# Kernel tuning notes

Measured on AMD Instinct MI355X. Metric: run time of the kernel, lower is better.

## Reference

```python
import jax, jax.numpy as jnp
import numpy as np

D_MODEL = 512
D_INNER = 1024   # expand * d_model
D_STATE = 16
D_CONV = 4
DT_RANK = 32     # ceil(d_model / 16)
BATCH = 8
SEQ = 1024


def _mamba(x, in_w, conv_w, conv_b, xp_w, dt_w, dt_b, A_log, Dp, out_w):
    # x: [B, L, d_model]
    Bb, Ls, _ = x.shape
    u, z = jnp.split(x @ in_w.T, 2, axis=-1)          # each [B, L, d_inner]
    # causal depthwise conv1d, kernel D_CONV, left-padded then truncated to L
    up = jnp.pad(u, ((0, 0), (D_CONV - 1, 0), (0, 0)))
    uc = conv_b + sum(up[:, k:k + Ls, :] * conv_w[:, k] for k in range(D_CONV))
    u = jax.nn.silu(uc)
    dbl = u @ xp_w.T                                   # [B, L, dt_rank+2*d_state]
    dt, Bm, Cm = jnp.split(dbl, [DT_RANK, DT_RANK + D_STATE], axis=-1)
    delta = jax.nn.softplus(dt @ dt_w.T + dt_b)        # [B, L, d_inner]
    A = -jnp.exp(A_log)                                # [d_inner, d_state]

    def step(h, inp):
        d_t, B_t, C_t, u_t = inp                       # [B,di],[B,ds],[B,ds],[B,di]
        h = h * jnp.exp(d_t[..., None] * A) + (d_t * u_t)[..., None] * B_t[:, None, :]
        return h, jnp.einsum('bds,bs->bd', h, C_t)

    h0 = jnp.zeros((Bb, D_INNER, D_STATE), x.dtype)
    xs = tuple(jnp.swapaxes(a, 0, 1) for a in (delta, Bm, Cm, u))
    _, ys = jax.lax.scan(step, h0, xs)                 # ys: [L, B, d_inner]
    y = jnp.swapaxes(ys, 0, 1) + u * Dp
    return (y * jax.nn.silu(z)) @ out_w.T              # [B, L, d_model]


def _params(key):
    ks = jax.random.split(key, 5)
    s = 0.02
    return {
        'in_w': jax.random.normal(ks[0], (2 * D_INNER, D_MODEL)) * s,
        'conv_w': jax.random.normal(ks[1], (D_INNER, D_CONV)) * 0.3,
        'conv_b': jnp.zeros((D_INNER,)),
        'xp_w': jax.random.normal(ks[2], (DT_RANK + 2 * D_STATE, D_INNER)) * s,
        'dt_w': jax.random.normal(ks[3], (D_INNER, DT_RANK)) * (DT_RANK ** -0.5),
        'dt_b': jnp.full((D_INNER,), -4.0),
        'A_log': jnp.log(jnp.tile(jnp.arange(1, D_STATE + 1, dtype=jnp.float32), (D_INNER, 1))),
        'D': jnp.ones((D_INNER,)),
        'out_w': jax.random.normal(ks[4], (D_MODEL, D_INNER)) * s,
    }


def setup_inputs():
    key = jax.random.key(0)
    kx, kf, kb = jax.random.split(key, 3)
    inp = {'x': jax.random.normal(kx, (BATCH, SEQ, D_MODEL), dtype=jnp.float32)}
    for n, v in _params(kf).items():
        inp[n + '_f'] = v
    for n, v in _params(kb).items():
        inp[n + '_b'] = v
    return inp


def reference(x, in_w_f, conv_w_f, conv_b_f, xp_w_f, dt_w_f, dt_b_f, A_log_f, D_f, out_w_f,
              in_w_b, conv_w_b, conv_b_b, xp_w_b, dt_w_b, dt_b_b, A_log_b, D_b, out_w_b):
    fwd = _mamba(x, in_w_f, conv_w_f, conv_b_f, xp_w_f, dt_w_f, dt_b_f, A_log_f, D_f, out_w_f)
    bwd = _mamba(x[:, ::-1, :], in_w_b, conv_w_b, conv_b_b, xp_w_b, dt_w_b, dt_b_b,
                 A_log_b, D_b, out_w_b)[:, ::-1, :]
    return fwd + bwd
```

## Files before the change

kernel.cpp:

```cpp
#include <hip/hip_runtime.h>
#include <math.h>

#define BATCH 8
#define SEQ 1024
#define D_MODEL 512
#define D_INNER 1024
#define D_STATE 16
#define DT_RANK 32
#define NROWS (BATCH * SEQ)
#define CH 64
#define CL 16
#define USLAB 8388608l

typedef short short8 __attribute__((ext_vector_type(8)));
typedef float f32x4 __attribute__((ext_vector_type(4)));

__device__ __forceinline__ float sigmoidf_(float x) { return 1.f / (1.f + __expf(-x)); }

__device__ __forceinline__ float softplus_(float v) {
  return (v > 20.f) ? v : __logf(1.f + __expf(v));
}

__device__ __forceinline__ ushort f2b(float f) {
  uint u = __float_as_uint(f);
  return (ushort)((u + 0x7FFFu + ((u >> 16) & 1u)) >> 16);
}
__device__ __forceinline__ float b2f(ushort u) {
  return __uint_as_float(((uint)u) << 16);
}

__device__ __forceinline__ void gload16(const ushort* g, const ushort* l) {
  __builtin_amdgcn_global_load_lds(
      (const __attribute__((address_space(1))) void*)g,
      (__attribute__((address_space(3))) void*)l, 16, 0, 0);
}

__device__ __forceinline__ int revrow(int m) {
  return (m & ~1023) | (1023 - (m & 1023));
}

__global__ __launch_bounds__(512, 2) void inproj256(
    const ushort* __restrict__ A, int lda,
    const ushort* __restrict__ B, int ldb,
    ushort* __restrict__ Cu, ushort* __restrict__ Cz,
    int K)
{
  __shared__ ushort As[3][256 * 32];
  __shared__ ushort Bs[3][256 * 32];
  const int tid = threadIdx.x;
  const int w = tid >> 6, lane = tid & 63;

  const int nwg = gridDim.x * gridDim.y;
  int bid = blockIdx.y * gridDim.x + blockIdx.x;
  int wgid = (bid & 7) * (nwg >> 3) + (bid >> 3);
  const int bm = (wgid / gridDim.x) * 256;
  const int bn = (wgid % gridDim.x) * 256;

  const int wr = w >> 2, wc = w & 3;
  const int rw0 = wr * 128, cw0 = wc * 64;
  const int srow = w * 16 + (lane >> 2);
  const int scol = (((lane & 3) ^ ((lane >> 3) & 3)) << 3);
  const int rchunk = (((lane >> 4) ^ (((lane & 15) >> 1) & 3)) << 3);

  f32x4 acc[8][4] = {};

  auto stageA = [&](int buf, int k0, int half) {
    int gm = bm + half * 128 + srow;
    gload16(A + (long)gm * lda + k0 + scol, &As[buf][(half * 128 + w * 16) * 32]);
  };
  auto stageB = [&](int buf, int k0, int half) {
    int gn = bn + half * 128 + srow;
    gload16(B + (long)gn * ldb + k0 + scol, &Bs[buf][(half * 128 + w * 16) * 32]);
  };

  const int NT = K >> 5;
  stageA(0, 0, 0); stageA(0, 0, 1); stageB(0, 0, 0); stageB(0, 0, 1);
  stageA(1, 32, 0); stageA(1, 32, 1); stageB(1, 32, 0); stageB(1, 32, 1);
  asm volatile("s_waitcnt vmcnt(4)" ::: "memory");
  __builtin_amdgcn_s_barrier();

  int buf = 0;
  for (int t = 0; t < NT; ++t) {
    const int kf = (t + 2) << 5;
    const int sbuf = (buf >= 1) ? buf - 1 : buf + 2;
    short8 a0[4], b0[4];
#pragma unroll
    for (int i = 0; i < 4; ++i)
      a0[i] = *(const short8*)&As[buf][(rw0 + i * 16 + (lane & 15)) * 32 + rchunk];
#pragma unroll
    for (int j = 0; j < 4; ++j)
      b0[j] = *(const short8*)&Bs[buf][(cw0 + j * 16 + (lane & 15)) * 32 + rchunk];
    if (t + 2 < NT) { stageA(sbuf, kf, 0); stageA(sbuf, kf, 1); }
    __builtin_amdgcn_s_barrier();
    __builtin_amdgcn_s_setprio(1);
#pragma unroll
    for (int i = 0; i < 4; ++i)
#pragma unroll
      for (int j = 0; j < 4; ++j)
        acc[i][j] = __builtin_amdgcn_mfma_f32_16x16x32_bf16(a0[i], b0[j], acc[i][j], 0, 0, 0);
    __builtin_amdgcn_s_setprio(0);
    __builtin_amdgcn_s_barrier();
    short8 a1[4];
#pragma unroll
    for (int i = 0; i < 4; ++i)
      a1[i] = *(const short8*)&As[buf][(rw0 + 64 + i * 16 + (lane & 15)) * 32 + rchunk];
    if (t + 2 < NT) {
      stageB(sbuf, kf, 0); stageB(sbuf, kf, 1);
      asm volatile("s_waitcnt vmcnt(4)" ::: "memory");
    } else if (t + 1 < NT) {
      asm volatile("s_waitcnt vmcnt(0)" ::: "memory");
    }
    __builtin_amdgcn_s_barrier();
    __builtin_amdgcn_s_setprio(1);
#pragma unroll
    for (int i = 0; i < 4; ++i)
#pragma unroll
      for (int j = 0; j < 4; ++j)
        acc[4 + i][j] = __builtin_amdgcn_mfma_f32_16x16x32_bf16(a1[i], b0[j], acc[4 + i][j], 0, 0, 0);
    __builtin_amdgcn_s_setprio(0);
    __builtin_amdgcn_s_barrier();
    buf = (buf == 2) ? 0 : buf + 1;
  }

  const int bdir = bn >> 11;
  const int bz = ((bn & 2047) >= 1024);
  const int bncol = bn & 1023;
  ushort* Cp = (bz ? Cz : Cu) + (long)bdir * USLAB;
  ushort* scr = &As[0][0] + w * 1024;

#pragma unroll
  for (int i = 0; i < 8; ++i) {
#pragma unroll
    for (int r = 0; r < 4; ++r)
#pragma unroll
      for (int j = 0; j < 4; ++j) {
        float v = acc[i][j][r];
        if (bz) v = v * sigmoidf_(v);
        scr[((lane >> 4) * 4 + r) * 64 + j * 16 + (lane & 15)] = f2b(v);
      }
#pragma unroll
    for (int q = 0; q < 2; ++q) {
      int r16 = (lane >> 3) + q * 8;
      short8 pk = *(const short8*)&scr[r16 * 64 + (lane & 7) * 8];
      int m = bm + rw0 + i * 16 + r16;
      int row = bdir ? revrow(m) : m;
      *(short8*)&Cp[(long)row * 1024 + bncol + cw0 + (lane & 7) * 8] = pk;
    }
  }
}

template<int BM, int BN, int RW, int CW, int EPI, int DUALK, int MDIAG>
__global__ __launch_bounds__(256) void gemm_bf16(
    const ushort* __restrict__ A, int lda, const ushort* __restrict__ A2,
    const ushort* __restrict__ B, int ldb, const ushort* __restrict__ B2,
    float* __restrict__ Cf, ushort* __restrict__ Cb, ushort* __restrict__ Cb2,
    int ldc, int K, const float* __restrict__ bias, const float* __restrict__ bias2,
    int b_stride, int revC, int accumC)
{
  constexpr int MI = BM / RW / 16;
  constexpr int NJ = BN / CW / 16;
  __shared__ ushort As[2][BM * 32];
  __shared__ ushort Bs[2][BN * 32];
  const int tid = threadIdx.x;
  const int w = tid >> 6, lane = tid & 63;

  const int nwg = gridDim.x * gridDim.y;
  int bid = blockIdx.y * gridDim.x + blockIdx.x;
  int wgid = (bid & 7) * (nwg >> 3) + (bid >> 3);
  const int bm = (wgid / gridDim.x) * BM;
  const int bn = (wgid % gridDim.x) * BN;

  if (MDIAG) {
    int mdir = (bm >= NROWS) ? 1 : 0;
    B += mdir * b_stride;
    if (mdir) bias = bias2;
  }

  const int rw0 = (w / CW) * (MI * 16);
  const int cw0 = (w % CW) * (NJ * 16);
  const int srow = w * 16 + (lane >> 2);
  const int scol = (((lane & 3) ^ ((lane >> 3) & 3)) << 3);
  const int rchunk = (((lane >> 4) ^ (((lane & 15) >> 1) & 3)) << 3);

  f32x4 acc[MI][NJ] = {};

  auto stage = [&](int buf, int k0) {
    const ushort* Ap = A;
    const ushort* Bp = B;
    int kc = k0;
    bool hi = false;
    if (DUALK && k0 >= (K >> 1)) { Ap = A2; Bp = B2; kc = k0 - (K >> 1); hi = true; }
#pragma unroll
    for (int it = 0; it < BM / 64; ++it) {
      int gm = bm + it * 64 + srow;
      int arow = (DUALK && hi) ? revrow(gm) : gm;
      gload16(Ap + (long)arow * lda + kc + scol, &As[buf][(it * 64 + w * 16) * 32]);
    }
#pragma unroll
    for (int it = 0; it < BN / 64; ++it) {
      int gn = bn + it * 64 + srow;
      gload16(Bp + (long)gn * ldb + kc + scol, &Bs[buf][(it * 64 + w * 16) * 32]);
    }
  };

  stage(0, 0);
  __syncthreads();

  for (int k0 = 0; k0 < K; k0 += 32) {
    int cur = (k0 >> 5) & 1;
    if (k0 + 32 < K) stage(cur ^ 1, k0 + 32);
    short8 a[MI], b[NJ];
#pragma unroll
    for (int i = 0; i < MI; ++i)
      a[i] = *(const short8*)&As[cur][(rw0 + i * 16 + (lane & 15)) * 32 + rchunk];
#pragma unroll
    for (int j = 0; j < NJ; ++j)
      b[j] = *(const short8*)&Bs[cur][(cw0 + j * 16 + (lane & 15)) * 32 + rchunk];
#pragma unroll
    for (int i = 0; i < MI; ++i)
#pragma unroll
      for (int j = 0; j < NJ; ++j)
        acc[i][j] = __builtin_amdgcn_mfma_f32_16x16x32_bf16(a[i], b[j], acc[i][j], 0, 0, 0);
    __syncthreads();
  }

  if (EPI == 1) {
    ushort* scr = &As[0][0] + w * 1024;
#pragma unroll
    for (int i = 0; i < MI; ++i) {
#pragma unroll
      for (int r = 0; r < 4; ++r)
#pragma unroll
        for (int j = 0; j < NJ; ++j) {
          int n = bn + cw0 + j * 16 + (lane & 15);
          float v = softplus_(acc[i][j][r] + bias[n]);
          scr[((lane >> 4) * 4 + r) * 64 + j * 16 + (lane & 15)] = f2b(v);
        }
#pragma unroll
      for (int q = 0; q < 2; ++q) {
        int r16 = (lane >> 3) + q * 8;
        short8 pk = *(const short8*)&scr[r16 * 64 + (lane & 7) * 8];
        int m = bm + rw0 + i * 16 + r16;
        *(short8*)&Cb[(long)m * ldc + bn + cw0 + (lane & 7) * 8] = pk;
      }
    }
  } else {
#pragma unroll
    for (int i = 0; i < MI; ++i)
#pragma unroll
      for (int r = 0; r < 4; ++r) {
        int m = bm + rw0 + i * 16 + (lane >> 4) * 4 + r;
        int crow = revC ? revrow(m) : m;
#pragma unroll
        for (int j = 0; j < NJ; ++j) {
          int n = bn + cw0 + j * 16 + (lane & 15);
          float v = acc[i][j][r];
          if (EPI == 0) {
            float* p = Cf + (long)crow * ldc + n;
            if (accumC) *p += v; else *p = v;
          } else {
            Cb[(long)crow * ldc + n] = f2b(v);
          }
        }
      }
  }
}

struct Seg { const float4* s; ushort4* d; int n4; int bstart; };
struct ConvArgs { Seg seg[9]; };

__global__ __launch_bounds__(256) void convert_all(ConvArgs a)
{
  int blk = blockIdx.x;
  int i = 0;
#pragma unroll
  for (int k = 1; k < 9; ++k) if (blk >= a.seg[k].bstart) i = k;
  int idx = (blk - a.seg[i].bstart) * 256 + threadIdx.x;
  if (idx >= a.seg[i].n4) return;
  float4 v = a.seg[i].s[idx];
  ushort4 o;
  o.x = f2b(v.x); o.y = f2b(v.y); o.z = f2b(v.z); o.w = f2b(v.w);
  a.seg[i].d[idx] = o;
}

__global__ __launch_bounds__(256) void conv_silu(
    const ushort* __restrict__ u_bf,
    const float* __restrict__ cw_f, const float* __restrict__ cw_b,
    const float* __restrict__ cb_f, const float* __restrict__ cb_b,
    ushort* __restrict__ uc_bf)
{
  long i = (long)blockIdx.x * 256 + threadIdx.x;
  int dir = (int)(i >> 21);
  int r = (int)(i >> 8) & 8191;
  int d0 = ((int)i & 255) << 2;
  int t = r & (SEQ - 1);
  const float* cw = dir ? cw_b : cw_f;
  const float* cb = dir ? cb_b : cb_f;
  const ushort* p = u_bf + dir * USLAB + (long)r * D_INNER + d0;
  ushort4 u0 = *(const ushort4*)p;
  ushort4 u1 = (t >= 1) ? *(const ushort4*)(p - 1024) : ushort4{0, 0, 0, 0};
  ushort4 u2 = (t >= 2) ? *(const ushort4*)(p - 2048) : ushort4{0, 0, 0, 0};
  ushort4 u3 = (t >= 3) ? *(const ushort4*)(p - 3072) : ushort4{0, 0, 0, 0};
  float4 bb = *(const float4*)(cb + d0);
  float ub0[4] = {b2f(u0.x), b2f(u0.y), b2f(u0.z), b2f(u0.w)};
  float ub1[4] = {b2f(u1.x), b2f(u1.y), b2f(u1.z), b2f(u1.w)};
  float ub2[4] = {b2f(u2.x), b2f(u2.y), b2f(u2.z), b2f(u2.w)};
  float ub3[4] = {b2f(u3.x), b2f(u3.y), b2f(u3.z), b2f(u3.w)};
  float bbv[4] = {bb.x, bb.y, bb.z, bb.w};
  ushort ov[4];
#pragma unroll
  for (int j = 0; j < 4; ++j) {
    float4 wj = *(const float4*)(cw + (d0 + j) * 4);
    float acc = bbv[j];
    acc = fmaf(wj.w, ub0[j], acc);
    acc = fmaf(wj.z, ub1[j], acc);
    acc = fmaf(wj.y, ub2[j], acc);
    acc = fmaf(wj.x, ub3[j], acc);
    ov[j] = f2b(acc * sigmoidf_(acc));
  }
  ushort4 o;
  o.x = ov[0]; o.y = ov[1]; o.z = ov[2]; o.w = ov[3];
  *(ushort4*)(uc_bf + dir * USLAB + (long)r * D_INNER + d0) = o;
}

#define EP_FAST(dt, Ep)                                        \
  {                                                            \
    float E1 = __expf(-(dt));                                  \
    float E2 = E1 * E1, E4 = E2 * E2, E8 = E4 * E4;            \
    Ep[0] = E1;  Ep[1] = E2;      Ep[2] = E2 * E1;             \
    Ep[3] = E4;  Ep[4] = E4 * E1; Ep[5] = E4 * E2;             \
    Ep[6] = E4 * Ep[2]; Ep[7] = E8;  Ep[8] = E8 * E1;          \
    Ep[9] = E8 * E2; Ep[10] = E8 * Ep[2]; Ep[11] = E8 * E4;    \
    Ep[12] = E8 * Ep[4]; Ep[13] = E8 * Ep[5];                  \
    Ep[14] = E8 * Ep[6]; Ep[15] = E8 * E8;                     \
  }

__device__ __forceinline__ bool a_is_arange(const float* Ar) {
  bool ok = true;
#pragma unroll
  for (int s = 0; s < D_STATE; ++s)
    ok = ok && (fabsf(Ar[s] + (float)(s + 1)) <= 1e-3f * (float)(s + 1));
  return ok;
}

__global__ __launch_bounds__(256) void scan_partA(
    const ushort* __restrict__ delta_bf,
    const ushort* __restrict__ ucv_bf,
    const ushort* __restrict__ dblb,
    const float* __restrict__ A_log_f, const float* __restrict__ A_log_b,
    ushort* __restrict__ hend,
    float* __restrict__ dtsum_buf)
{
  __shared__ float bc[CL][16];
  long idx = (long)blockIdx.x * 256 + threadIdx.x;
  int d = (int)idx & 1023;
  int c = ((int)idx >> 10) & (CH - 1);
  int b = ((int)idx >> 16) & 7;
  int dir = (int)(idx >> 19);
  const long r0 = (long)b * SEQ + c * CL;
  const ushort* dblp = dblb + (long)dir * NROWS * 64;
  {
    int tt = threadIdx.x >> 4, ss = threadIdx.x & 15;
    bc[tt][ss] = b2f(dblp[(r0 + tt) * 64 + 32 + ss]);
  }
  const float* Alog = dir ? A_log_b : A_log_f;
  const ushort* dp = delta_bf + dir * USLAB;
  const ushort* up = ucv_bf + dir * USLAB;
  float Ar[D_STATE];
#pragma unroll
  for (int s = 0; s < D_STATE; ++s) Ar[s] = -__expf(Alog[d * D_STATE + s]);
  const bool fast = a_is_arange(Ar);
  float h[D_STATE] = {0.f};
  float dtsum = 0.f;
  __syncthreads();

  if (fast) {
    for (int t = 0; t < CL; ++t) {
      long r = r0 + t;
      float dt = b2f(dp[r * 1024 + d]);
      float u  = b2f(up[r * 1024 + d]);
      float du = dt * u;
      dtsum += dt;
      float Ep[16];
      EP_FAST(dt, Ep);
#pragma unroll
      for (int s = 0; s < D_STATE; ++s)
        h[s] = fmaf(h[s], Ep[s], du * bc[t][s]);
    }
  } else {
    for (int t = 0; t < CL; ++t) {
      long r = r0 + t;
      float dt = b2f(dp[r * 1024 + d]);
      float u  = b2f(up[r * 1024 + d]);
      float du = dt * u;
      dtsum += dt;
#pragma unroll
      for (int s = 0; s < D_STATE; ++s)
        h[s] = fmaf(h[s], __expf(dt * Ar[s]), du * bc[t][s]);
    }
  }
  long base = ((long)((dir * 8 + b) * CH + c) * D_STATE) * 1024 + d;
#pragma unroll
  for (int s = 0; s < D_STATE; ++s) hend[base + s * 1024] = f2b(h[s]);
  dtsum_buf[(long)((dir * 8 + b) * CH + c) * 1024 + d] = dtsum;
}

__global__ __launch_bounds__(256) void scan_partB(
    ushort* __restrict__ hend,
    const float* __restrict__ dtsum_buf,
    const float* __restrict__ A_log_f, const float* __restrict__ A_log_b)
{
  long idx = (long)blockIdx.x * 256 + threadIdx.x;
  int d = (int)idx & 1023;
  int s = ((int)idx >> 10) & 15;
  int b = ((int)idx >> 14) & 7;
  int dir = (int)(idx >> 17);
  const float* Alog = dir ? A_log_b : A_log_f;
  float Ars = -__expf(Alog[d * D_STATE + s]);
  float H = 0.f;
  for (int c = 0; c < CH; ++c) {
    long off = ((long)((dir * 8 + b) * CH + c) * D_STATE + s) * 1024 + d;
    float he = b2f(hend[off]);
    float P = __expf(Ars * dtsum_buf[(long)((dir * 8 + b) * CH + c) * 1024 + d]);
    hend[off] = f2b(H);
    H = fmaf(P, H, he);
  }
}

__global__ __launch_bounds__(256) void scan_partC(
    const ushort* __restrict__ delta_bf,
    const ushort* __restrict__ ucv_bf,
    const ushort* __restrict__ dblb,
    const float* __restrict__ A_log_f, const float* __restrict__ A_log_b,
    const float* __restrict__ Dp_f, const float* __restrict__ Dp_b,
    const ushort* __restrict__ zsilu_bf,
    const ushort* __restrict__ hinit,
    ushort* __restrict__ ydz_bf)
{
  __shared__ float bc[CL][32];
  long idx = (long)blockIdx.x * 256 + threadIdx.x;
  int d = (int)idx & 1023;
  int c = ((int)idx >> 10) & (CH - 1);
  int b = ((int)idx >> 16) & 7;
  int dir = (int)(idx >> 19);
  const long r0 = (long)b * SEQ + c * CL;
  const ushort* dblp = dblb + (long)dir * NROWS * 64;
  {
    int tt = threadIdx.x >> 4, cc = (threadIdx.x & 15) * 2;
    ushort2 v = *(const ushort2*)&dblp[(r0 + tt) * 64 + 32 + cc];
    bc[tt][cc] = b2f(v.x); bc[tt][cc + 1] = b2f(v.y);
  }
  const float* Alog = dir ? A_log_b : A_log_f;
  const ushort* dp = delta_bf + dir * USLAB;
  const ushort* up = ucv_bf + dir * USLAB;
  const ushort* zp = zsilu_bf + dir * USLAB;
  ushort* yp = ydz_bf + dir * USLAB;
  float Ar[D_STATE];
#pragma unroll
  for (int s = 0; s < D_STATE; ++s) Ar[s] = -__expf(Alog[d * D_STATE + s]);
  const bool fast = a_is_arange(Ar);
  float h[D_STATE];
  long base = ((long)((dir * 8 + b) * CH + c) * D_STATE) * 1024 + d;
#pragma unroll
  for (int s = 0; s < D_STATE; ++s) h[s] = b2f(hinit[base + s * 1024]);
  float Dd = (dir ? Dp_b : Dp_f)[d];
  __syncthreads();

  if (fast) {
    for (int t = 0; t < CL; ++t) {
      long r = r0 + t;
      float dt = b2f(dp[r * 1024 + d]);
      float u  = b2f(up[r * 1024 + d]);
      float du = dt * u;
      float Ep[16];
      EP_FAST(dt, Ep);
      float y = 0.f;
#pragma unroll
      for (int s = 0; s < D_STATE; ++s) {
        h[s] = fmaf(h[s], Ep[s], du * bc[t][s]);
        y = fmaf(h[s], bc[t][16 + s], y);
      }
      float zs = b2f(zp[r * 1024 + d]);
      float yv = fmaf(u, Dd, y);
      yp[r * 1024 + d] = f2b(yv * zs);
    }
  } else {
    for (int t = 0; t < CL; ++t) {
      long r = r0 + t;
      float dt = b2f(dp[r * 1024 + d]);
      float u  = b2f(up[r * 1024 + d]);
      float du = dt * u;
      float y = 0.f;
#pragma unroll
      for (int s = 0; s < D_STATE; ++s) {
        h[s] = fmaf(h[s], __expf(dt * Ar[s]), du * bc[t][s]);
        y = fmaf(h[s], bc[t][16 + s], y);
      }
      float zs = b2f(zp[r * 1024 + d]);
      float yv = fmaf(u, Dd, y);
      yp[r * 1024 + d] = f2b(yv * zs);
    }
  }
}

extern "C" void kernel_launch(void* const* d_in, const int* in_sizes, int n_in,
                              void* d_out, int out_size, void* d_ws, size_t ws_size,
                              hipStream_t stream)
{
  const float* x = (const float*)d_in[0];
  float* out = (float*)d_out;
  char* ws = (char*)d_ws;
  ushort* zsilu  = (ushort*)(ws);
  ushort* ucv    = (ushort*)(ws + (32ul << 20));
  ushort* u_bf   = (ushort*)(ws + (64ul << 20));
  ushort* hend   = (ushort*)(ws + (96ul << 20));
  float*  dtsum  = (float*)(ws + (128ul << 20));
  ushort* dblb   = (ushort*)(ws + (132ul << 20));
  ushort* out_wb = (ushort*)(ws + (134ul << 20));
  ushort* xbf    = hend;
  ushort* in_wb  = hend + (8ul << 19);
  ushort* xp_wb  = hend + (12ul << 19);
  ushort* dt_wb  = xp_wb + 131072;
  ushort* delta  = u_bf;
  ushort* ydz    = ucv;

  ConvArgs ca;
  int bcur = 0, si = 0;
  auto addseg = [&](const float* s, ushort* d, int nelem) {
    ca.seg[si].s = (const float4*)s; ca.seg[si].d = (ushort4*)d;
    ca.seg[si].n4 = nelem / 4; ca.seg[si].bstart = bcur;
    bcur += (nelem / 4 + 255) / 256; ++si;
  };
  addseg(x, xbf, NROWS * D_MODEL);
  addseg((const float*)d_in[1], in_wb, 2048 * 512);
  addseg((const float*)d_in[10], in_wb + 2048 * 512, 2048 * 512);
  addseg((const float*)d_in[9], out_wb, 512 * 1024);
  addseg((const float*)d_in[18], out_wb + 512 * 1024, 512 * 1024);
  addseg((const float*)d_in[4], xp_wb, 64 * 1024);
  addseg((const float*)d_in[13], xp_wb + 65536, 64 * 1024);
  addseg((const float*)d_in[5], dt_wb, 1024 * 32);
  addseg((const float*)d_in[14], dt_wb + 32768, 1024 * 32);

  dim3 blk(256);
  convert_all<<<dim3(bcur), blk, 0, stream>>>(ca);

  inproj256<<<dim3(4096 / 256, NROWS / 256), dim3(512), 0, stream>>>(
      xbf, D_MODEL, in_wb, D_MODEL, u_bf, zsilu, D_MODEL);
  conv_silu<<<dim3(2 * NROWS), blk, 0, stream>>>(
      u_bf, (const float*)d_in[2], (const float*)d_in[11],
      (const float*)d_in[3], (const float*)d_in[12], ucv);
  gemm_bf16<64, 64, 2, 2, 4, 0, 1><<<dim3(1, 256), blk, 0, stream>>>(
      ucv, D_INNER, nullptr, xp_wb, D_INNER, nullptr,
      nullptr, dblb, nullptr, 64, D_INNER, nullptr, nullptr, 65536, 0, 0);
  gemm_bf16<128, 128, 2, 2, 1, 0, 1><<<dim3(8, 128), blk, 0, stream>>>(
      dblb, 64, nullptr, dt_wb, DT_RANK, nullptr,
      nullptr, delta, nullptr, D_INNER, DT_RANK,
      (const float*)d_in[6], (const float*)d_in[15], 32768, 0, 0);
  const float* Alf = (const float*)d_in[7];
  const float* Alb = (const float*)d_in[16];
  scan_partA<<<dim3(2 * BATCH * CH * 1024 / 256), blk, 0, stream>>>(
      delta, ucv, dblb, Alf, Alb, hend, dtsum);
  scan_partB<<<dim3(2 * BATCH * 16 * 1024 / 256), blk, 0, stream>>>(
      hend, dtsum, Alf, Alb);
  scan_partC<<<dim3(2 * BATCH * CH * 1024 / 256), blk, 0, stream>>>(
      delta, ucv, dblb, Alf, Alb,
      (const float*)d_in[8], (const float*)d_in[17], zsilu, hend, ydz);
  gemm_bf16<128, 128, 2, 2, 0, 1, 0><<<dim3(4, 64), blk, 0, stream>>>(
      ydz, D_INNER, ydz + USLAB, out_wb, D_INNER, out_wb + 512 * 1024,
      out, nullptr, nullptr, D_MODEL, 2 * D_INNER, nullptr, nullptr, 0, 0, 0);
}
```

Before: 254.7 us.

## Fuse x_proj and dt_proj GEMMs into one kernel; widen conv_silu vectors

Adds xdt_kernel, which computes the x_proj GEMM for a 64-row tile, keeps the resulting dt/B/C tile in shared memory, and applies the dt projection with the softplus-plus-bias epilogue in the same kernel. Only B/C columns go to dblb; the dt columns are no longer written to and re-read from global memory, and one launch is saved. conv_silu now handles 8 channels per thread with short8 loads and stores instead of 4. The trade-off is that the fused kernel runs only 256 workgroups, each doing the whole dt projection serially across its 4 waves, which may reduce parallelism compared with the separate 1024-block delta GEMM.

```diff
diff --git a/kernel.cpp b/kernel.cpp
--- a/kernel.cpp
+++ b/kernel.cpp
@@ -149,6 +149,114 @@
   }
 }
 
+__global__ __launch_bounds__(256) void xdt_kernel(
+    const ushort* __restrict__ A,
+    const ushort* __restrict__ xp_w,
+    const ushort* __restrict__ dt_w,
+    const float* __restrict__ dt_b_f, const float* __restrict__ dt_b_b,
+    ushort* __restrict__ dblb,
+    ushort* __restrict__ delta)
+{
+  __shared__ ushort As[2][64 * 32];
+  __shared__ ushort Bs[2][64 * 32];
+  __shared__ ushort dblS[64][72];
+  __shared__ ushort scr[4][1024];
+  const int tid = threadIdx.x;
+  const int w = tid >> 6, lane = tid & 63;
+
+  const int nwg = gridDim.x;
+  int wgid = (blockIdx.x & 7) * (nwg >> 3) + (blockIdx.x >> 3);
+  const int bm = wgid * 64;
+  const int mdir = (bm >= NROWS) ? 1 : 0;
+  const ushort* B = xp_w + mdir * 65536;
+  const ushort* dtw = dt_w + mdir * 32768;
+  const float* dbias = mdir ? dt_b_b : dt_b_f;
+
+  const int rw0 = (w >> 1) * 32;
+  const int cw0 = (w & 1) * 32;
+  const int srow = w * 16 + (lane >> 2);
+  const int scol = (((lane & 3) ^ ((lane >> 3) & 3)) << 3);
+  const int rchunk = (((lane >> 4) ^ (((lane & 15) >> 1) & 3)) << 3);
+
+  f32x4 acc[2][2] = {};
+  auto stage = [&](int buf, int k0) {
+    gload16(A + (long)(bm + srow) * 1024 + k0 + scol, &As[buf][(w * 16) * 32]);
+    gload16(B + (long)srow * 1024 + k0 + scol, &Bs[buf][(w * 16) * 32]);
+  };
+  stage(0, 0);
+  __syncthreads();
+  for (int k0 = 0; k0 < 1024; k0 += 32) {
+    int cur = (k0 >> 5) & 1;
+    if (k0 + 32 < 1024) stage(cur ^ 1, k0 + 32);
+    short8 a[2], b[2];
+#pragma unroll
+    for (int i = 0; i < 2; ++i)
+      a[i] = *(const short8*)&As[cur][(rw0 + i * 16 + (lane & 15)) * 32 + rchunk];
+#pragma unroll
+    for (int j = 0; j < 2; ++j)
+      b[j] = *(const short8*)&Bs[cur][(cw0 + j * 16 + (lane & 15)) * 32 + rchunk];
+#pragma unroll
+    for (int i = 0; i < 2; ++i)
+#pragma unroll
+      for (int j = 0; j < 2; ++j)
+        acc[i][j] = __builtin_amdgcn_mfma_f32_16x16x32_bf16(a[i], b[j], acc[i][j], 0, 0, 0);
+    __syncthreads();
+  }
+
+#pragma unroll
+  for (int i = 0; i < 2; ++i)
+#pragma unroll
+    for (int r = 0; r < 4; ++r)
+#pragma unroll
+      for (int j = 0; j < 2; ++j)
+        dblS[rw0 + i * 16 + (lane >> 4) * 4 + r][cw0 + j * 16 + (lane & 15)] =
+            f2b(acc[i][j][r]);
+  __syncthreads();
+
+  {
+    int row = tid >> 2, cg = tid & 3;
+    short8 pk = *(const short8*)&dblS[row][32 + cg * 8];
+    *(short8*)&dblb[(long)(bm + row) * 64 + 32 + cg * 8] = pk;
+  }
+
+  for (int g = 0; g < 4; ++g) {
+    int n0 = w * 256 + g * 64;
+    short8 a2[4], b2[4];
+#pragma unroll
+    for (int m = 0; m < 4; ++m)
+      a2[m] = *(const short8*)&dblS[m * 16 + (lane & 15)][(lane >> 4) * 8];
+#pragma unroll
+    for (int j = 0; j < 4; ++j)
+      b2[j] = *(const short8*)&dtw[(long)(n0 + j * 16 + (lane & 15)) * 32 + (lane >> 4) * 8];
+    f32x4 acc2[4][4] = {};
+#pragma unroll
+    for (int m = 0; m < 4; ++m)
+#pragma unroll
+      for (int j = 0; j < 4; ++j)
+        acc2[m][j] = __builtin_amdgcn_mfma_f32_16x16x32_bf16(a2[m], b2[j], acc2[m][j], 0, 0, 0);
+    float bv[4];
+#pragma unroll
+    for (int j = 0; j < 4; ++j) bv[j] = dbias[n0 + j * 16 + (lane & 15)];
+#pragma unroll
+    for (int m = 0; m < 4; ++m) {
+#pragma unroll
+      for (int r = 0; r < 4; ++r)
+#pragma unroll
+        for (int j = 0; j < 4; ++j) {
+          float v = softplus_(acc2[m][j][r] + bv[j]);
+          scr[w][((lane >> 4) * 4 + r) * 64 + j * 16 + (lane & 15)] = f2b(v);
+        }
+#pragma unroll
+      for (int q = 0; q < 2; ++q) {
+        int r16 = (lane >> 3) + q * 8;
+        short8 pk = *(const short8*)&scr[w][r16 * 64 + (lane & 7) * 8];
+        int grow = bm + m * 16 + r16;
+        *(short8*)&delta[(long)grow * 1024 + n0 + (lane & 7) * 8] = pk;
+      }
+    }
+  }
+}
+
 template<int BM, int BN, int RW, int CW, int EPI, int DUALK, int MDIAG>
 __global__ __launch_bounds__(256) void gemm_bf16(
     const ushort* __restrict__ A, int lda, const ushort* __restrict__ A2,
@@ -224,46 +332,24 @@
     __syncthreads();
   }
 
-  if (EPI == 1) {
-    ushort* scr = &As[0][0] + w * 1024;
-#pragma unroll
-    for (int i = 0; i < MI; ++i) {
-#pragma unroll
-      for (int r = 0; r < 4; ++r)
-#pragma unroll
-        for (int j = 0; j < NJ; ++j) {
-          int n = bn + cw0 + j * 16 + (lane & 15);
-          float v = softplus_(acc[i][j][r] + bias[n]);
-          scr[((lane >> 4) * 4 + r) * 64 + j * 16 + (lane & 15)] = f2b(v);
-        }
-#pragma unroll
-      for (int q = 0; q < 2; ++q) {
-        int r16 = (lane >> 3) + q * 8;
-        short8 pk = *(const short8*)&scr[r16 * 64 + (lane & 7) * 8];
-        int m = bm + rw0 + i * 16 + r16;
-        *(short8*)&Cb[(long)m * ldc + bn + cw0 + (lane & 7) * 8] = pk;
-      }
-    }
-  } else {
-#pragma unroll
-    for (int i = 0; i < MI; ++i)
-#pragma unroll
-      for (int r = 0; r < 4; ++r) {
-        int m = bm + rw0 + i * 16 + (lane >> 4) * 4 + r;
-        int crow = revC ? revrow(m) : m;
-#pragma unroll
-        for (int j = 0; j < NJ; ++j) {
-          int n = bn + cw0 + j * 16 + (lane & 15);
-          float v = acc[i][j][r];
-          if (EPI == 0) {
-            float* p = Cf + (long)crow * ldc + n;
-            if (accumC) *p += v; else *p = v;
-          } else {
-            Cb[(long)crow * ldc + n] = f2b(v);
-          }
+#pragma unroll
+  for (int i = 0; i < MI; ++i)
+#pragma unroll
+    for (int r = 0; r < 4; ++r) {
+      int m = bm + rw0 + i * 16 + (lane >> 4) * 4 + r;
+      int crow = revC ? revrow(m) : m;
+#pragma unroll
+      for (int j = 0; j < NJ; ++j) {
+        int n = bn + cw0 + j * 16 + (lane & 15);
+        float v = acc[i][j][r];
+        if (EPI == 0) {
+          float* p = Cf + (long)crow * ldc + n;
+          if (accumC) *p += v; else *p = v;
+        } else {
+          Cb[(long)crow * ldc + n] = f2b(v);
         }
       }
-  }
+    }
 }
 
 struct Seg { const float4* s; ushort4* d; int n4; int bstart; };
@@ -290,37 +376,33 @@
     ushort* __restrict__ uc_bf)
 {
   long i = (long)blockIdx.x * 256 + threadIdx.x;
-  int dir = (int)(i >> 21);
-  int r = (int)(i >> 8) & 8191;
-  int d0 = ((int)i & 255) << 2;
+  int dir = (int)(i >> 20);
+  int r = (int)(i >> 7) & 8191;
+  int d0 = ((int)i & 127) << 3;
   int t = r & (SEQ - 1);
   const float* cw = dir ? cw_b : cw_f;
   const float* cb = dir ? cb_b : cb_f;
   const ushort* p = u_bf + dir * USLAB + (long)r * D_INNER + d0;
-  ushort4 u0 = *(const ushort4*)p;
-  ushort4 u1 = (t >= 1) ? *(const ushort4*)(p - 1024) : ushort4{0, 0, 0, 0};
-  ushort4 u2 = (t >= 2) ? *(const ushort4*)(p - 2048) : ushort4{0, 0, 0, 0};
-  ushort4 u3 = (t >= 3) ? *(const ushort4*)(p - 3072) : ushort4{0, 0, 0, 0};
-  float4 bb = *(const float4*)(cb + d0);
-  float ub0[4] = {b2f(u0.x), b2f(u0.y), b2f(u0.z), b2f(u0.w)};
-  float ub1[4] = {b2f(u1.x), b2f(u1.y), b2f(u1.z), b2f(u1.w)};
-  float ub2[4] = {b2f(u2.x), b2f(u2.y), b2f(u2.z), b2f(u2.w)};
-  float ub3[4] = {b2f(u3.x), b2f(u3.y), b2f(u3.z), b2f(u3.w)};
-  float bbv[4] = {bb.x, bb.y, bb.z, bb.w};
-  ushort ov[4];
-#pragma unroll
-  for (int j = 0; j < 4; ++j) {
+  short8 z8 = {0, 0, 0, 0, 0, 0, 0, 0};
+  short8 u0 = *(const short8*)p;
+  short8 u1 = (t >= 1) ? *(const short8*)(p - 1024) : z8;
+  short8 u2 = (t >= 2) ? *(const short8*)(p - 2048) : z8;
+  short8 u3 = (t >= 3) ? *(const short8*)(p - 3072) : z8;
+  float4 bb0 = *(const float4*)(cb + d0);
+  float4 bb1 = *(const float4*)(cb + d0 + 4);
+  float bbv[8] = {bb0.x, bb0.y, bb0.z, bb0.w, bb1.x, bb1.y, bb1.z, bb1.w};
+  short8 o;
+#pragma unroll
+  for (int j = 0; j < 8; ++j) {
     float4 wj = *(const float4*)(cw + (d0 + j) * 4);
     float acc = bbv[j];
-    acc = fmaf(wj.w, ub0[j], acc);
-    acc = fmaf(wj.z, ub1[j], acc);
-    acc = fmaf(wj.y, ub2[j], acc);
-    acc = fmaf(wj.x, ub3[j], acc);
-    ov[j] = f2b(acc * sigmoidf_(acc));
-  }
-  ushort4 o;
-  o.x = ov[0]; o.y = ov[1]; o.z = ov[2]; o.w = ov[3];
-  *(ushort4*)(uc_bf + dir * USLAB + (long)r * D_INNER + d0) = o;
+    acc = fmaf(wj.w, b2f((ushort)u0[j]), acc);
+    acc = fmaf(wj.z, b2f((ushort)u1[j]), acc);
+    acc = fmaf(wj.y, b2f((ushort)u2[j]), acc);
+    acc = fmaf(wj.x, b2f((ushort)u3[j]), acc);
+    o[j] = (short)f2b(acc * sigmoidf_(acc));
+  }
+  *(short8*)(uc_bf + dir * USLAB + (long)r * D_INNER + d0) = o;
 }
 
 #define EP_FAST(dt, Ep)                                        \
@@ -546,16 +628,12 @@
 
   inproj256<<<dim3(4096 / 256, NROWS / 256), dim3(512), 0, stream>>>(
       xbf, D_MODEL, in_wb, D_MODEL, u_bf, zsilu, D_MODEL);
-  conv_silu<<<dim3(2 * NROWS), blk, 0, stream>>>(
+  conv_silu<<<dim3(2 * NROWS * D_INNER / 8 / 256), blk, 0, stream>>>(
       u_bf, (const float*)d_in[2], (const float*)d_in[11],
       (const float*)d_in[3], (const float*)d_in[12], ucv);
-  gemm_bf16<64, 64, 2, 2, 4, 0, 1><<<dim3(1, 256), blk, 0, stream>>>(
-      ucv, D_INNER, nullptr, xp_wb, D_INNER, nullptr,
-      nullptr, dblb, nullptr, 64, D_INNER, nullptr, nullptr, 65536, 0, 0);
-  gemm_bf16<128, 128, 2, 2, 1, 0, 1><<<dim3(8, 128), blk, 0, stream>>>(
-      dblb, 64, nullptr, dt_wb, DT_RANK, nullptr,
-      nullptr, delta, nullptr, D_INNER, DT_RANK,
-      (const float*)d_in[6], (const float*)d_in[15], 32768, 0, 0);
+  xdt_kernel<<<dim3(256), blk, 0, stream>>>(
+      ucv, xp_wb, dt_wb, (const float*)d_in[6], (const float*)d_in[15],
+      dblb, delta);
   const float* Alf = (const float*)d_in[7];
   const float* Alb = (const float*)d_in[16];
   scan_partA<<<dim3(2 * BATCH * CH * 1024 / 256), blk, 0, stream>>>(
```

New measurement: 264.6 us. 3.9% more time.

## Shrink in-projection GEMM tile to 256x128 and raise occupancy

Applied to the files above, without the earlier changes.

The in-projection GEMM tile shrinks from 256x256 to 256x128. Each of the 8 waves now computes a 64x64 sub-tile with 16 accumulators instead of 32, and the launch bound allows 4 workgroups per CU instead of 2. The pipeline is simplified to one staging call and one MFMA phase per K step, which removes two of the three barriers in each iteration. The aim is more blocks and waves in flight to hide latency. The cost is lower data reuse per block, so global and LDS traffic for the A operand doubles.

```diff
diff --git a/kernel.cpp b/kernel.cpp
--- a/kernel.cpp
+++ b/kernel.cpp
@@ -39,14 +39,14 @@
   return (m & ~1023) | (1023 - (m & 1023));
 }
 
-__global__ __launch_bounds__(512, 2) void inproj256(
+__global__ __launch_bounds__(512, 4) void inproj256(
     const ushort* __restrict__ A, int lda,
     const ushort* __restrict__ B, int ldb,
     ushort* __restrict__ Cu, ushort* __restrict__ Cz,
     int K)
 {
   __shared__ ushort As[3][256 * 32];
-  __shared__ ushort Bs[3][256 * 32];
+  __shared__ ushort Bs[3][128 * 32];
   const int tid = threadIdx.x;
   const int w = tid >> 6, lane = tid & 63;
 
@@ -54,73 +54,59 @@
   int bid = blockIdx.y * gridDim.x + blockIdx.x;
   int wgid = (bid & 7) * (nwg >> 3) + (bid >> 3);
   const int bm = (wgid / gridDim.x) * 256;
-  const int bn = (wgid % gridDim.x) * 256;
-
-  const int wr = w >> 2, wc = w & 3;
-  const int rw0 = wr * 128, cw0 = wc * 64;
+  const int bn = (wgid % gridDim.x) * 128;
+
+  const int wr = w >> 1, wc = w & 1;
+  const int rw0 = wr * 64, cw0 = wc * 64;
   const int srow = w * 16 + (lane >> 2);
   const int scol = (((lane & 3) ^ ((lane >> 3) & 3)) << 3);
   const int rchunk = (((lane >> 4) ^ (((lane & 15) >> 1) & 3)) << 3);
 
-  f32x4 acc[8][4] = {};
-
-  auto stageA = [&](int buf, int k0, int half) {
-    int gm = bm + half * 128 + srow;
-    gload16(A + (long)gm * lda + k0 + scol, &As[buf][(half * 128 + w * 16) * 32]);
+  f32x4 acc[4][4] = {};
+
+  auto stage = [&](int buf, int k0) {
+#pragma unroll
+    for (int half = 0; half < 2; ++half) {
+      int gm = bm + half * 128 + srow;
+      gload16(A + (long)gm * lda + k0 + scol, &As[buf][(half * 128 + w * 16) * 32]);
+    }
+    int gn = bn + srow;
+    gload16(B + (long)gn * ldb + k0 + scol, &Bs[buf][(w * 16) * 32]);
   };
-  auto stageB = [&](int buf, int k0, int half) {
-    int gn = bn + half * 128 + srow;
-    gload16(B + (long)gn * ldb + k0 + scol, &Bs[buf][(half * 128 + w * 16) * 32]);
-  };
 
   const int NT = K >> 5;
-  stageA(0, 0, 0); stageA(0, 0, 1); stageB(0, 0, 0); stageB(0, 0, 1);
-  stageA(1, 32, 0); stageA(1, 32, 1); stageB(1, 32, 0); stageB(1, 32, 1);
-  asm volatile("s_waitcnt vmcnt(4)" ::: "memory");
+  stage(0, 0);
+  stage(1, 32);
+  asm volatile("s_waitcnt vmcnt(3)" ::: "memory");
   __builtin_amdgcn_s_barrier();
 
   int buf = 0;
   for (int t = 0; t < NT; ++t) {
-    const int kf = (t + 2) << 5;
-    const int sbuf = (buf >= 1) ? buf - 1 : buf + 2;
-    short8 a0[4], b0[4];
+    short8 a[4], b[4];
 #pragma unroll
     for (int i = 0; i < 4; ++i)
-      a0[i] = *(const short8*)&As[buf][(rw0 + i * 16 + (lane & 15)) * 32 + rchunk];
+      a[i] = *(const short8*)&As[buf][(rw0 + i * 16 + (lane & 15)) * 32 + rchunk];
 #pragma unroll
     for (int j = 0; j < 4; ++j)
-      b0[j] = *(const short8*)&Bs[buf][(cw0 + j * 16 + (lane & 15)) * 32 + rchunk];
-    if (t + 2 < NT) { stageA(sbuf, kf, 0); stageA(sbuf, kf, 1); }
+      b[j] = *(const short8*)&Bs[buf][(cw0 + j * 16 + (lane & 15)) * 32 + rchunk];
+    int sbuf = (buf >= 1) ? buf - 1 : buf + 2;
+    if (t + 2 < NT) {
+      stage(sbuf, (t + 2) << 5);
+      asm volatile("s_waitcnt vmcnt(3)" ::: "memory");
+    } else if (t + 1 < NT) {
+      asm volatile("s_waitcnt vmcnt(0)" ::: "memory");
+    }
     __builtin_amdgcn_s_barrier();
     __builtin_amdgcn_s_setprio(1);
 #pragma unroll
     for (int i = 0; i < 4; ++i)
 #pragma unroll
       for (int j = 0; j < 4; ++j)
-        acc[i][j] = __builtin_amdgcn_mfma_f32_16x16x32_bf16(a0[i], b0[j], acc[i][j], 0, 0, 0);
+        acc[i][j] = __builtin_amdgcn_mfma_f32_16x16x32_bf16(a[i], b[j], acc[i][j], 0, 0, 0);
     __builtin_amdgcn_s_setprio(0);
-    __builtin_amdgcn_s_barrier();
-    short8 a1[4];
-#pragma unroll
-    for (int i = 0; i < 4; ++i)
-      a1[i] = *(const short8*)&As[buf][(rw0 + 64 + i * 16 + (lane & 15)) * 32 + rchunk];
-    if (t + 2 < NT) {
-      stageB(sbuf, kf, 0); stageB(sbuf, kf, 1);
-      asm volatile("s_waitcnt vmcnt(4)" ::: "memory");
-    } else if (t + 1 < NT) {
-      asm volatile("s_waitcnt vmcnt(0)" ::: "memory");
-    }
-    __builtin_amdgcn_s_barrier();
-    __builtin_amdgcn_s_setprio(1);
-#pragma unroll
-    for (int i = 0; i < 4; ++i)
-#pragma unroll
-      for (int j = 0; j < 4; ++j)
-        acc[4 + i][j] = __builtin_amdgcn_mfma_f32_16x16x32_bf16(a1[i], b0[j], acc[4 + i][j], 0, 0, 0);
-    __builtin_amdgcn_s_setprio(0);
-    __builtin_amdgcn_s_barrier();
     buf = (buf == 2) ? 0 : buf + 1;
   }
+  __builtin_amdgcn_s_barrier();
 
   const int bdir = bn >> 11;
   const int bz = ((bn & 2047) >= 1024);
@@ -129,7 +115,7 @@
   ushort* scr = &As[0][0] + w * 1024;
 
 #pragma unroll
-  for (int i = 0; i < 8; ++i) {
+  for (int i = 0; i < 4; ++i) {
 #pragma unroll
     for (int r = 0; r < 4; ++r)
 #pragma unroll
@@ -544,7 +530,7 @@
   dim3 blk(256);
   convert_all<<<dim3(bcur), blk, 0, stream>>>(ca);
 
-  inproj256<<<dim3(4096 / 256, NROWS / 256), dim3(512), 0, stream>>>(
+  inproj256<<<dim3(4096 / 128, NROWS / 256), dim3(512), 0, stream>>>(
       xbf, D_MODEL, in_wb, D_MODEL, u_bf, zsilu, D_MODEL);
   conv_silu<<<dim3(2 * NROWS), blk, 0, stream>>>(
       u_bf, (const float*)d_in[2], (const float*)d_in[11],
```

After: 247.3 us. -2.9%, faster.
